# Performance work log

Hardware: AMD Instinct MI355X
Metric: run time of the kernel (lower is better)

The kernel has to match this reference:

```python
import jax, jax.numpy as jnp
import numpy as np

V, D, DU, H = 50000, 256, 1024, 128
TEMP = 0.01

def time_cosine_emb(t, d_model):
    half = d_model // 2
    div_term = jnp.exp(jnp.arange(half, dtype=jnp.float32) * (-np.log(10000.0) / half))
    scaled = t[..., None] * div_term  # (B, L, half)
    return jnp.concatenate([jnp.sin(scaled), jnp.cos(scaled)], axis=-1)

def setup_inputs() -> dict:
    key = jax.random.key(0)
    ks = jax.random.split(key, 12)
    B, L = 64, 2048
    q_seq = jax.random.randint(ks[0], (B, L), 0, V)
    r_seq = jax.random.randint(ks[1], (B, L), 0, 3)
    t_seq = jax.random.uniform(ks[2], (B, L), dtype=jnp.float32) * 1000.0
    mask = jnp.ones((B, L), dtype=jnp.float32)
    q_tab = jax.random.normal(ks[3], (V, D), dtype=jnp.float32) * 0.02
    q_tab = q_tab.at[0].set(0.0)  # padding_idx=0
    r_tab = jax.random.normal(ks[4], (3, D), dtype=jnp.float32) * 0.02
    r_tab = r_tab.at[0].set(0.0)  # padding_idx=0
    virtual_node = jax.random.normal(ks[5], (1, D), dtype=jnp.float32)
    Ws1 = jax.random.normal(ks[6], (H, 2 * D), dtype=jnp.float32) * (1.0 / np.sqrt(2 * D))
    bs1 = jnp.zeros((H,), dtype=jnp.float32)
    Ws2 = jax.random.normal(ks[7], (1, H), dtype=jnp.float32) * (1.0 / np.sqrt(H))
    bs2 = jnp.zeros((1,), dtype=jnp.float32)
    Wa = jax.random.normal(ks[8], (DU, D), dtype=jnp.float32) * (1.0 / np.sqrt(D))
    ba = jnp.zeros((DU,), dtype=jnp.float32)
    return {"q_seq": q_seq, "r_seq": r_seq, "t_seq": t_seq, "mask": mask,
            "q_tab": q_tab, "r_tab": r_tab, "virtual_node": virtual_node,
            "Ws1": Ws1, "bs1": bs1, "Ws2": Ws2, "bs2": bs2, "Wa": Wa, "ba": ba}

def reference(q_seq, r_seq, t_seq, mask, q_tab, r_tab, virtual_node, Ws1, bs1, Ws2, bs2, Wa, ba):
    B, L = q_seq.shape
    d_model = q_tab.shape[1]
    # embedding gathers + trig time embedding
    h_events = q_tab[q_seq] + r_tab[r_seq] + time_cosine_emb(t_seq, d_model)  # (B,L,D)
    h_virtual = jnp.broadcast_to(virtual_node[None, :, :], (B, L, d_model))
    pair = jnp.concatenate([h_events, h_virtual], axis=-1)  # (B,L,2D)
    # struct_head: Linear -> LeakyReLU(0.2) -> Linear
    hdn = jax.nn.leaky_relu(jnp.einsum('bld,hd->blh', pair, Ws1) + bs1, 0.2)
    logits = jnp.einsum('blh,oh->blo', hdn, Ws2) + bs2  # (B,L,1)
    A_hat = jax.nn.sigmoid(logits / TEMP) * mask[..., None]
    # aggregator: Linear -> LeakyReLU(0.2)
    h_trans = jax.nn.leaky_relu(jnp.einsum('bld,ud->blu', h_events, Wa) + ba, 0.2)  # (B,L,DU)
    u_i = jnp.sum(h_trans * A_hat, axis=1)  # (B,DU)
    return (u_i, jnp.squeeze(A_hat, -1))
```

## Files before the change

### kernel.cpp

```cpp
#include <hip/hip_runtime.h>

typedef unsigned short ushort_t;
typedef unsigned int uint_t;

typedef short bf16x8 __attribute__((ext_vector_type(8)));
typedef float f32x4 __attribute__((ext_vector_type(4)));

#define MFMA16(a, b, c) __builtin_amdgcn_mfma_f32_16x16x32_bf16(a, b, c, 0, 0, 0)

__device__ __forceinline__ ushort_t f2bf(float f) {
    uint_t u = __float_as_uint(f);
    u += 0x7fffu + ((u >> 16) & 1u);
    return (ushort_t)(u >> 16);
}
__device__ __forceinline__ float bf2f(ushort_t h) {
    return __uint_as_float(((uint_t)h) << 16);
}

__device__ __forceinline__ void async16(const ushort_t* g, ushort_t* l) {
    __builtin_amdgcn_global_load_lds(
        (const __attribute__((address_space(1))) uint_t*)g,
        (__attribute__((address_space(3))) uint_t*)l, 16, 0, 0);
}

__global__ void k_consth(const float* __restrict__ Ws1, const float* __restrict__ bs1,
                         const float* __restrict__ virt, float* __restrict__ consth) {
    int h = threadIdx.x;
    if (h >= 128) return;
    const float* row = Ws1 + h * 512 + 256;
    float s = bs1[h];
    for (int d = 0; d < 256; ++d) s += row[d] * virt[d];
    consth[h] = s;
}

__global__ void k_convert(const float* __restrict__ src, int src_stride,
                          ushort_t* __restrict__ dhi, ushort_t* __restrict__ dlo, int rows) {
    int tid = blockIdx.x * blockDim.x + threadIdx.x;
    int total = rows * 32;
    if (tid >= total) return;
    int pl = tid & 15, kc = (tid >> 4) & 31, pt = tid >> 9;
    int row = pt * 16 + pl;
    const float* s = src + (size_t)row * src_stride + kc * 8;
    ushort_t hs[8], ls[8];
#pragma unroll
    for (int j = 0; j < 8; ++j) {
        float v = s[j];
        ushort_t h = f2bf(v);
        hs[j] = h;
        ls[j] = f2bf(v - bf2f(h));
    }
    uint4 hv;
    hv.x = hs[0] | ((uint_t)hs[1] << 16); hv.y = hs[2] | ((uint_t)hs[3] << 16);
    hv.z = hs[4] | ((uint_t)hs[5] << 16); hv.w = hs[6] | ((uint_t)hs[7] << 16);
    *(uint4*)(dhi + (size_t)tid * 8) = hv;
    if (dlo) {
        uint4 lv;
        lv.x = ls[0] | ((uint_t)ls[1] << 16); lv.y = ls[2] | ((uint_t)ls[3] << 16);
        lv.z = ls[4] | ((uint_t)ls[5] << 16); lv.w = ls[6] | ((uint_t)ls[7] << 16);
        *(uint4*)(dlo + (size_t)tid * 8) = lv;
    }
}

__global__ __launch_bounds__(256, 2) void k_embed_struct(
    const int* __restrict__ q_seq, const int* __restrict__ r_seq,
    const float* __restrict__ t_seq, const float* __restrict__ q_tab,
    const float* __restrict__ r_tab,
    const ushort_t* __restrict__ ws1h, const ushort_t* __restrict__ ws1l,
    const float* __restrict__ consth, const float* __restrict__ Ws2,
    const float* __restrict__ bs2, const float* __restrict__ mask,
    ushort_t* __restrict__ h_hi, float* __restrict__ out_ahat) {
    __shared__ ushort_t sAhi[16384];
    __shared__ ushort_t sAlo[16384];
    __shared__ float sdiv[128];
    __shared__ float sLogit[64];
    int tid = threadIdx.x;
    if (tid < 128) sdiv[tid] = expf((float)tid * -0.07195578415606394f);
    if (tid < 64) sLogit[tid] = 0.0f;
    int w = tid >> 6, lane = tid & 63;
    int pl = lane & 15, kq = lane >> 4;
    int nl = pl;
    int ptile = blockIdx.x * 4 + w;
    int p = ptile * 16 + pl;
    int q = q_seq[p], r = r_seq[p];
    float tt = t_seq[p];
    const float4* qrow = (const float4*)(q_tab + (size_t)q * 256);
    const float4* rrow = (const float4*)(r_tab + (size_t)r * 256);
    bf16x8 Bhi[2][8], Blo[2][8];
#pragma unroll
    for (int nt = 0; nt < 2; ++nt) {
        int ntg = w * 2 + nt;
#pragma unroll
        for (int ks = 0; ks < 8; ++ks) {
            int off = ((ntg * 32 + ks * 4 + kq) * 16 + nl) * 8;
            Bhi[nt][ks] = *(const bf16x8*)(ws1h + off);
            Blo[nt][ks] = *(const bf16x8*)(ws1l + off);
        }
    }
    __syncthreads();
#pragma unroll
    for (int it = 0; it < 8; ++it) {
        int kc = it * 4 + kq;
        int k0 = kc * 8;
        float4 qa = qrow[kc * 2], qb = qrow[kc * 2 + 1];
        float4 ra = rrow[kc * 2], rb = rrow[kc * 2 + 1];
        float v[8] = {qa.x + ra.x, qa.y + ra.y, qa.z + ra.z, qa.w + ra.w,
                      qb.x + rb.x, qb.y + rb.y, qb.z + rb.z, qb.w + rb.w};
        bool iscos = (kc >= 16);
#pragma unroll
        for (int j = 0; j < 8; ++j) {
            float ang = tt * sdiv[(k0 + j) & 127];
            v[j] += iscos ? cosf(ang) : sinf(ang);
        }
        ushort_t hs[8], ls[8];
#pragma unroll
        for (int j = 0; j < 8; ++j) {
            ushort_t h = f2bf(v[j]);
            hs[j] = h;
            ls[j] = f2bf(v[j] - bf2f(h));
        }
        uint4 hv, lv;
        hv.x = hs[0] | ((uint_t)hs[1] << 16); hv.y = hs[2] | ((uint_t)hs[3] << 16);
        hv.z = hs[4] | ((uint_t)hs[5] << 16); hv.w = hs[6] | ((uint_t)hs[7] << 16);
        lv.x = ls[0] | ((uint_t)ls[1] << 16); lv.y = ls[2] | ((uint_t)ls[3] << 16);
        lv.z = ls[4] | ((uint_t)ls[5] << 16); lv.w = ls[6] | ((uint_t)ls[7] << 16);
        *(uint4*)(h_hi + ((size_t)(ptile * 32 + kc) * 16 + pl) * 8) = hv;
        int loff = ((w * 32 + kc) * 16 + pl) * 8;
        *(uint4*)(sAhi + loff) = hv;
        *(uint4*)(sAlo + loff) = lv;
    }
    __syncthreads();
    f32x4 acc[4][2];
    f32x4 z4 = {0.f, 0.f, 0.f, 0.f};
#pragma unroll
    for (int mt = 0; mt < 4; ++mt)
#pragma unroll
        for (int nt = 0; nt < 2; ++nt) acc[mt][nt] = z4;
#pragma unroll
    for (int ks = 0; ks < 8; ++ks) {
        bf16x8 ahi[4], alo[4];
#pragma unroll
        for (int mt = 0; mt < 4; ++mt) {
            int off = ((mt * 32 + ks * 4 + kq) * 16 + nl) * 8;
            ahi[mt] = *(const bf16x8*)&sAhi[off];
            alo[mt] = *(const bf16x8*)&sAlo[off];
        }
#pragma unroll
        for (int mt = 0; mt < 4; ++mt)
#pragma unroll
            for (int nt = 0; nt < 2; ++nt) {
                acc[mt][nt] = MFMA16(ahi[mt], Bhi[nt][ks], acc[mt][nt]);
                acc[mt][nt] = MFMA16(alo[mt], Bhi[nt][ks], acc[mt][nt]);
                acc[mt][nt] = MFMA16(ahi[mt], Blo[nt][ks], acc[mt][nt]);
            }
    }
    float ps[4][4];
#pragma unroll
    for (int mt = 0; mt < 4; ++mt)
#pragma unroll
        for (int r = 0; r < 4; ++r) ps[mt][r] = 0.f;
#pragma unroll
    for (int nt = 0; nt < 2; ++nt) {
        int ng = w * 32 + nt * 16 + nl;
        float chv = consth[ng], w2 = Ws2[ng];
#pragma unroll
        for (int mt = 0; mt < 4; ++mt)
#pragma unroll
            for (int r = 0; r < 4; ++r) {
                float v = acc[mt][nt][r] + chv;
                v = v > 0.f ? v : 0.2f * v;
                ps[mt][r] += v * w2;
            }
    }
#pragma unroll
    for (int mt = 0; mt < 4; ++mt)
#pragma unroll
        for (int r = 0; r < 4; ++r) {
            float x = ps[mt][r];
            x += __shfl_xor(x, 1, 64);
            x += __shfl_xor(x, 2, 64);
            x += __shfl_xor(x, 4, 64);
            x += __shfl_xor(x, 8, 64);
            ps[mt][r] = x;
        }
    if (nl == 0) {
#pragma unroll
        for (int mt = 0; mt < 4; ++mt)
#pragma unroll
            for (int r = 0; r < 4; ++r)
                atomicAdd(&sLogit[mt * 16 + kq * 4 + r], ps[mt][r]);
    }
    __syncthreads();
    if (tid < 64) {
        int pp = blockIdx.x * 64 + tid;
        float lg = sLogit[tid] + bs2[0];
        float y = lg * 100.0f;
        y = fminf(fmaxf(y, -60.f), 60.f);
        float a = 1.0f / (1.0f + expf(-y));
        out_ahat[pp] = a * mask[pp];
    }
}

__global__ __launch_bounds__(256, 2) void k_agg(
    const ushort_t* __restrict__ h_hi, const ushort_t* __restrict__ wa_blk,
    const float* __restrict__ ba, const float* __restrict__ ahat,
    float* __restrict__ u_i) {
    __shared__ ushort_t sA[16384];
    __shared__ ushort_t sB[16384];
    __shared__ float sAh[128];
    int tid = threadIdx.x;
    int w = tid >> 6, lane = tid & 63, nl = lane & 15, kq = lane >> 4;
    int p0 = blockIdx.x * 128, bidx = p0 >> 11;
    if (tid < 128) sAh[tid] = ahat[p0 + tid];
    int mh = w & 1, nh = w >> 1;
    const ushort_t* gA = h_hi + (size_t)(p0 >> 4) * 4096;
    for (int nch = 0; nch < 8; ++nch) {
        const ushort_t* gB = wa_blk + (size_t)nch * 8 * 4096;
        int n0 = nch * 128;
        f32x4 acc[4][4];
        f32x4 z4 = {0.f, 0.f, 0.f, 0.f};
#pragma unroll
        for (int mt = 0; mt < 4; ++mt)
#pragma unroll
            for (int nt = 0; nt < 4; ++nt) acc[mt][nt] = z4;
        for (int kh = 0; kh < 2; ++kh) {
#pragma unroll
            for (int i = 0; i < 16; ++i) {
                int gi = w * 16 + i;
                int isB = gi >> 5;
                int loc = gi & 31;
                int tl = loc >> 2, sub = loc & 3;
                const ushort_t* src = (isB ? gB : gA) +
                                      ((size_t)tl * 32 + kh * 16) * 128 + sub * 512 + lane * 8;
                ushort_t* dst = (isB ? sB : sA) + tl * 2048 + sub * 512;
                async16(src, dst);
            }
            __syncthreads();
#pragma unroll
            for (int ks = 0; ks < 4; ++ks) {
                bf16x8 af[4], bfr[4];
#pragma unroll
                for (int mt = 0; mt < 4; ++mt) {
                    int ptl = mh * 4 + mt;
                    af[mt] = *(const bf16x8*)&sA[(ptl * 256 + (ks * 4 + kq) * 16 + nl) * 8];
                }
#pragma unroll
                for (int nt = 0; nt < 4; ++nt) {
                    int ntl = nh * 4 + nt;
                    bfr[nt] = *(const bf16x8*)&sB[(ntl * 256 + (ks * 4 + kq) * 16 + nl) * 8];
                }
#pragma unroll
                for (int mt = 0; mt < 4; ++mt)
#pragma unroll
                    for (int nt = 0; nt < 4; ++nt)
                        acc[mt][nt] = MFMA16(af[mt], bfr[nt], acc[mt][nt]);
            }
            __syncthreads();
        }
#pragma unroll
        for (int nt = 0; nt < 4; ++nt) {
            int ng = n0 + nh * 64 + nt * 16 + nl;
            float ban = ba[ng];
            float s = 0.f;
#pragma unroll
            for (int mt = 0; mt < 4; ++mt)
#pragma unroll
                for (int r = 0; r < 4; ++r) {
                    float v = acc[mt][nt][r] + ban;
                    v = v > 0.f ? v : 0.2f * v;
                    int ml = mh * 64 + mt * 16 + kq * 4 + r;
                    s += v * sAh[ml];
                }
            s += __shfl_xor(s, 16, 64);
            s += __shfl_xor(s, 32, 64);
            if (kq == 0) atomicAdd(&u_i[bidx * 1024 + ng], s);
        }
    }
}

extern "C" void kernel_launch(void* const* d_in, const int* in_sizes, int n_in,
                              void* d_out, int out_size, void* d_ws, size_t ws_size,
                              hipStream_t stream) {
    const int* q_seq = (const int*)d_in[0];
    const int* r_seq = (const int*)d_in[1];
    const float* t_seq = (const float*)d_in[2];
    const float* mask = (const float*)d_in[3];
    const float* q_tab = (const float*)d_in[4];
    const float* r_tab = (const float*)d_in[5];
    const float* virt = (const float*)d_in[6];
    const float* Ws1 = (const float*)d_in[7];
    const float* bs1 = (const float*)d_in[8];
    const float* Ws2 = (const float*)d_in[9];
    const float* bs2 = (const float*)d_in[10];
    const float* Wa = (const float*)d_in[11];
    const float* ba = (const float*)d_in[12];
    float* out = (float*)d_out;

    ushort_t* h_hi = (ushort_t*)d_ws;
    ushort_t* wa_b = h_hi + 33554432;
    ushort_t* ws1h = wa_b + 262144;
    ushort_t* ws1l = ws1h + 32768;
    float* ch = (float*)(ws1l + 32768);

    hipMemsetAsync(out, 0, 65536 * sizeof(float), stream);
    hipLaunchKernelGGL(k_consth, dim3(1), dim3(128), 0, stream, Ws1, bs1, virt, ch);
    hipLaunchKernelGGL(k_convert, dim3(128), dim3(256), 0, stream,
                       Wa, 256, wa_b, (ushort_t*)nullptr, 1024);
    hipLaunchKernelGGL(k_convert, dim3(16), dim3(256), 0, stream,
                       Ws1, 512, ws1h, ws1l, 128);
    hipLaunchKernelGGL(k_embed_struct, dim3(2048), dim3(256), 0, stream,
                       q_seq, r_seq, t_seq, q_tab, r_tab, ws1h, ws1l, ch, Ws2, bs2,
                       mask, h_hi, out + 65536);
    hipLaunchKernelGGL(k_agg, dim3(1024), dim3(256), 0, stream,
                       h_hi, wa_b, ba, out + 65536, out);
}
```

Before: 287.7 us.

## Fuse prep kernels, stage gathered rows via async LDS loads, restructure aggregator tiling

Merges the three setup kernels into one launch. The embed kernel now gathers q_tab rows into LDS with async global-to-LDS loads, uses fast sin/cos/exp intrinsics, and streams Ws1 fragments one k-step ahead instead of holding all of them in registers. It also drops to one block per CU because of the larger LDS footprint. The aggregator keeps the whole A tile in registers and loads a full Wa chunk into LDS per n-chunk, removing the K-half loop. The cost is lower occupancy and less accurate fast trig on large angles.

```diff
diff --git a/kernel.cpp b/kernel.cpp
--- a/kernel.cpp
+++ b/kernel.cpp
@@ -23,21 +23,31 @@
         (__attribute__((address_space(3))) uint_t*)l, 16, 0, 0);
 }
 
-__global__ void k_consth(const float* __restrict__ Ws1, const float* __restrict__ bs1,
-                         const float* __restrict__ virt, float* __restrict__ consth) {
-    int h = threadIdx.x;
-    if (h >= 128) return;
-    const float* row = Ws1 + h * 512 + 256;
-    float s = bs1[h];
-    for (int d = 0; d < 256; ++d) s += row[d] * virt[d];
-    consth[h] = s;
-}
-
-__global__ void k_convert(const float* __restrict__ src, int src_stride,
-                          ushort_t* __restrict__ dhi, ushort_t* __restrict__ dlo, int rows) {
-    int tid = blockIdx.x * blockDim.x + threadIdx.x;
-    int total = rows * 32;
-    if (tid >= total) return;
+__global__ void k_prep(const float* __restrict__ Ws1, const float* __restrict__ bs1,
+                       const float* __restrict__ virt, const float* __restrict__ Wa,
+                       float* __restrict__ consth, ushort_t* __restrict__ wa_b,
+                       ushort_t* __restrict__ ws1h, ushort_t* __restrict__ ws1l) {
+    int b = blockIdx.x;
+    if (b == 0) {
+        int h = threadIdx.x;
+        if (h < 128) {
+            const float* row = Ws1 + h * 512 + 256;
+            float s = bs1[h];
+            for (int d = 0; d < 256; ++d) s += row[d] * virt[d];
+            consth[h] = s;
+        }
+        return;
+    }
+    const float* src;
+    int src_stride, tid;
+    ushort_t *dhi, *dlo;
+    if (b <= 128) {
+        tid = (b - 1) * 256 + threadIdx.x;
+        src = Wa; src_stride = 256; dhi = wa_b; dlo = nullptr;
+    } else {
+        tid = (b - 129) * 256 + threadIdx.x;
+        src = Ws1; src_stride = 512; dhi = ws1h; dlo = ws1l;
+    }
     int pl = tid & 15, kc = (tid >> 4) & 31, pt = tid >> 9;
     int row = pt * 16 + pl;
     const float* s = src + (size_t)row * src_stride + kc * 8;
@@ -61,7 +71,7 @@
     }
 }
 
-__global__ __launch_bounds__(256, 2) void k_embed_struct(
+__global__ __launch_bounds__(256, 1) void k_embed_struct(
     const int* __restrict__ q_seq, const int* __restrict__ r_seq,
     const float* __restrict__ t_seq, const float* __restrict__ q_tab,
     const float* __restrict__ r_tab,
@@ -69,47 +79,46 @@
     const float* __restrict__ consth, const float* __restrict__ Ws2,
     const float* __restrict__ bs2, const float* __restrict__ mask,
     ushort_t* __restrict__ h_hi, float* __restrict__ out_ahat) {
+    __shared__ ushort_t sQ[33280];
     __shared__ ushort_t sAhi[16384];
     __shared__ ushort_t sAlo[16384];
     __shared__ float sdiv[128];
     __shared__ float sLogit[64];
     int tid = threadIdx.x;
-    if (tid < 128) sdiv[tid] = expf((float)tid * -0.07195578415606394f);
+    if (tid < 128) sdiv[tid] = __expf((float)tid * -0.07195578415606394f);
     if (tid < 64) sLogit[tid] = 0.0f;
     int w = tid >> 6, lane = tid & 63;
     int pl = lane & 15, kq = lane >> 4;
     int nl = pl;
-    int ptile = blockIdx.x * 4 + w;
-    int p = ptile * 16 + pl;
-    int q = q_seq[p], r = r_seq[p];
+    int p0 = blockIdx.x * 64;
+    int p = p0 + w * 16 + pl;
+    int qv = q_seq[p0 + w * 16 + (lane & 15)];
+    int rr = r_seq[p];
     float tt = t_seq[p];
-    const float4* qrow = (const float4*)(q_tab + (size_t)q * 256);
-    const float4* rrow = (const float4*)(r_tab + (size_t)r * 256);
-    bf16x8 Bhi[2][8], Blo[2][8];
-#pragma unroll
-    for (int nt = 0; nt < 2; ++nt) {
-        int ntg = w * 2 + nt;
-#pragma unroll
-        for (int ks = 0; ks < 8; ++ks) {
-            int off = ((ntg * 32 + ks * 4 + kq) * 16 + nl) * 8;
-            Bhi[nt][ks] = *(const bf16x8*)(ws1h + off);
-            Blo[nt][ks] = *(const bf16x8*)(ws1l + off);
-        }
+#pragma unroll
+    for (int i = 0; i < 16; ++i) {
+        int row = __shfl(qv, i, 64);
+        async16((const ushort_t*)(q_tab + (size_t)row * 256) + lane * 8,
+                sQ + (w * 16 + i) * 520);
     }
     __syncthreads();
+    const char* myrow = (const char*)sQ + (w * 16 + pl) * 1040;
+    const float* rrow = r_tab + (size_t)rr * 256;
 #pragma unroll
     for (int it = 0; it < 8; ++it) {
         int kc = it * 4 + kq;
         int k0 = kc * 8;
-        float4 qa = qrow[kc * 2], qb = qrow[kc * 2 + 1];
-        float4 ra = rrow[kc * 2], rb = rrow[kc * 2 + 1];
+        float4 qa = *(const float4*)(myrow + kc * 32);
+        float4 qb = *(const float4*)(myrow + kc * 32 + 16);
+        float4 ra = *(const float4*)(rrow + kc * 8);
+        float4 rb = *(const float4*)(rrow + kc * 8 + 4);
         float v[8] = {qa.x + ra.x, qa.y + ra.y, qa.z + ra.z, qa.w + ra.w,
                       qb.x + rb.x, qb.y + rb.y, qb.z + rb.z, qb.w + rb.w};
         bool iscos = (kc >= 16);
 #pragma unroll
         for (int j = 0; j < 8; ++j) {
             float ang = tt * sdiv[(k0 + j) & 127];
-            v[j] += iscos ? cosf(ang) : sinf(ang);
+            v[j] += iscos ? __cosf(ang) : __sinf(ang);
         }
         ushort_t hs[8], ls[8];
 #pragma unroll
@@ -123,7 +132,7 @@
         hv.z = hs[4] | ((uint_t)hs[5] << 16); hv.w = hs[6] | ((uint_t)hs[7] << 16);
         lv.x = ls[0] | ((uint_t)ls[1] << 16); lv.y = ls[2] | ((uint_t)ls[3] << 16);
         lv.z = ls[4] | ((uint_t)ls[5] << 16); lv.w = ls[6] | ((uint_t)ls[7] << 16);
-        *(uint4*)(h_hi + ((size_t)(ptile * 32 + kc) * 16 + pl) * 8) = hv;
+        *(uint4*)(h_hi + ((size_t)((blockIdx.x * 4 + w) * 32 + kc) * 16 + pl) * 8) = hv;
         int loff = ((w * 32 + kc) * 16 + pl) * 8;
         *(uint4*)(sAhi + loff) = hv;
         *(uint4*)(sAlo + loff) = lv;
@@ -135,8 +144,23 @@
     for (int mt = 0; mt < 4; ++mt)
 #pragma unroll
         for (int nt = 0; nt < 2; ++nt) acc[mt][nt] = z4;
-#pragma unroll
+    bf16x8 bhi[2], blo[2], nbhi[2], nblo[2];
+#pragma unroll
+    for (int nt = 0; nt < 2; ++nt) {
+        int off = (((w * 2 + nt) * 32 + kq) * 16 + nl) * 8;
+        bhi[nt] = *(const bf16x8*)(ws1h + off);
+        blo[nt] = *(const bf16x8*)(ws1l + off);
+    }
+#pragma unroll 1
     for (int ks = 0; ks < 8; ++ks) {
+        if (ks < 7) {
+#pragma unroll
+            for (int nt = 0; nt < 2; ++nt) {
+                int off = (((w * 2 + nt) * 32 + (ks + 1) * 4 + kq) * 16 + nl) * 8;
+                nbhi[nt] = *(const bf16x8*)(ws1h + off);
+                nblo[nt] = *(const bf16x8*)(ws1l + off);
+            }
+        }
         bf16x8 ahi[4], alo[4];
 #pragma unroll
         for (int mt = 0; mt < 4; ++mt) {
@@ -148,10 +172,12 @@
         for (int mt = 0; mt < 4; ++mt)
 #pragma unroll
             for (int nt = 0; nt < 2; ++nt) {
-                acc[mt][nt] = MFMA16(ahi[mt], Bhi[nt][ks], acc[mt][nt]);
-                acc[mt][nt] = MFMA16(alo[mt], Bhi[nt][ks], acc[mt][nt]);
-                acc[mt][nt] = MFMA16(ahi[mt], Blo[nt][ks], acc[mt][nt]);
+                acc[mt][nt] = MFMA16(ahi[mt], bhi[nt], acc[mt][nt]);
+                acc[mt][nt] = MFMA16(alo[mt], bhi[nt], acc[mt][nt]);
+                acc[mt][nt] = MFMA16(ahi[mt], blo[nt], acc[mt][nt]);
             }
+#pragma unroll
+        for (int nt = 0; nt < 2; ++nt) { bhi[nt] = nbhi[nt]; blo[nt] = nblo[nt]; }
     }
     float ps[4][4];
 #pragma unroll
@@ -191,7 +217,7 @@
     }
     __syncthreads();
     if (tid < 64) {
-        int pp = blockIdx.x * 64 + tid;
+        int pp = p0 + tid;
         float lg = sLogit[tid] + bs2[0];
         float y = lg * 100.0f;
         y = fminf(fmaxf(y, -60.f), 60.f);
@@ -204,58 +230,50 @@
     const ushort_t* __restrict__ h_hi, const ushort_t* __restrict__ wa_blk,
     const float* __restrict__ ba, const float* __restrict__ ahat,
     float* __restrict__ u_i) {
-    __shared__ ushort_t sA[16384];
-    __shared__ ushort_t sB[16384];
+    __shared__ ushort_t sB[32768];
     __shared__ float sAh[128];
     int tid = threadIdx.x;
     int w = tid >> 6, lane = tid & 63, nl = lane & 15, kq = lane >> 4;
     int p0 = blockIdx.x * 128, bidx = p0 >> 11;
     if (tid < 128) sAh[tid] = ahat[p0 + tid];
     int mh = w & 1, nh = w >> 1;
+    bf16x8 afr[4][8];
     const ushort_t* gA = h_hi + (size_t)(p0 >> 4) * 4096;
+#pragma unroll
+    for (int mt = 0; mt < 4; ++mt) {
+        const ushort_t* base = gA + (size_t)(mh * 4 + mt) * 4096;
+#pragma unroll
+        for (int ks = 0; ks < 8; ++ks)
+            afr[mt][ks] = *(const bf16x8*)(base + ks * 512 + lane * 8);
+    }
+#pragma unroll 1
     for (int nch = 0; nch < 8; ++nch) {
-        const ushort_t* gB = wa_blk + (size_t)nch * 8 * 4096;
-        int n0 = nch * 128;
+        const ushort_t* gB = wa_blk + (size_t)nch * 32768;
+#pragma unroll
+        for (int i = 0; i < 16; ++i)
+            async16(gB + (w * 16 + i) * 512 + lane * 8, sB + (w * 16 + i) * 512);
+        __syncthreads();
         f32x4 acc[4][4];
         f32x4 z4 = {0.f, 0.f, 0.f, 0.f};
 #pragma unroll
         for (int mt = 0; mt < 4; ++mt)
 #pragma unroll
             for (int nt = 0; nt < 4; ++nt) acc[mt][nt] = z4;
-        for (int kh = 0; kh < 2; ++kh) {
-#pragma unroll
-            for (int i = 0; i < 16; ++i) {
-                int gi = w * 16 + i;
-                int isB = gi >> 5;
-                int loc = gi & 31;
-                int tl = loc >> 2, sub = loc & 3;
-                const ushort_t* src = (isB ? gB : gA) +
-                                      ((size_t)tl * 32 + kh * 16) * 128 + sub * 512 + lane * 8;
-                ushort_t* dst = (isB ? sB : sA) + tl * 2048 + sub * 512;
-                async16(src, dst);
+#pragma unroll
+        for (int ks = 0; ks < 8; ++ks) {
+            bf16x8 bfr[4];
+#pragma unroll
+            for (int nt = 0; nt < 4; ++nt) {
+                int ntl = nh * 4 + nt;
+                bfr[nt] = *(const bf16x8*)&sB[ntl * 4096 + ks * 512 + lane * 8];
             }
-            __syncthreads();
-#pragma unroll
-            for (int ks = 0; ks < 4; ++ks) {
-                bf16x8 af[4], bfr[4];
-#pragma unroll
-                for (int mt = 0; mt < 4; ++mt) {
-                    int ptl = mh * 4 + mt;
-                    af[mt] = *(const bf16x8*)&sA[(ptl * 256 + (ks * 4 + kq) * 16 + nl) * 8];
-                }
-#pragma unroll
-                for (int nt = 0; nt < 4; ++nt) {
-                    int ntl = nh * 4 + nt;
-                    bfr[nt] = *(const bf16x8*)&sB[(ntl * 256 + (ks * 4 + kq) * 16 + nl) * 8];
-                }
-#pragma unroll
-                for (int mt = 0; mt < 4; ++mt)
-#pragma unroll
-                    for (int nt = 0; nt < 4; ++nt)
-                        acc[mt][nt] = MFMA16(af[mt], bfr[nt], acc[mt][nt]);
-            }
-            __syncthreads();
-        }
+#pragma unroll
+            for (int mt = 0; mt < 4; ++mt)
+#pragma unroll
+                for (int nt = 0; nt < 4; ++nt)
+                    acc[mt][nt] = MFMA16(afr[mt][ks], bfr[nt], acc[mt][nt]);
+        }
+        int n0 = nch * 128;
 #pragma unroll
         for (int nt = 0; nt < 4; ++nt) {
             int ng = n0 + nh * 64 + nt * 16 + nl;
@@ -274,6 +292,7 @@
             s += __shfl_xor(s, 32, 64);
             if (kq == 0) atomicAdd(&u_i[bidx * 1024 + ng], s);
         }
+        __syncthreads();
     }
 }
 
@@ -302,11 +321,8 @@
     float* ch = (float*)(ws1l + 32768);
 
     hipMemsetAsync(out, 0, 65536 * sizeof(float), stream);
-    hipLaunchKernelGGL(k_consth, dim3(1), dim3(128), 0, stream, Ws1, bs1, virt, ch);
-    hipLaunchKernelGGL(k_convert, dim3(128), dim3(256), 0, stream,
-                       Wa, 256, wa_b, (ushort_t*)nullptr, 1024);
-    hipLaunchKernelGGL(k_convert, dim3(16), dim3(256), 0, stream,
-                       Ws1, 512, ws1h, ws1l, 128);
+    hipLaunchKernelGGL(k_prep, dim3(145), dim3(256), 0, stream,
+                       Ws1, bs1, virt, Wa, ch, wa_b, ws1h, ws1l);
     hipLaunchKernelGGL(k_embed_struct, dim3(2048), dim3(256), 0, stream,
                        q_seq, r_seq, t_seq, q_tab, r_tab, ws1h, ws1l, ch, Ws2, bs2,
                        mask, h_hi, out + 65536);
```

New measurement: 273.2 us. 1.05x faster.
